# Optimization experiments

Measured on AMD Instinct MI355X. Metric: run time of the kernel, lower is better.

## Reference

```python
import jax, jax.numpy as jnp
import numpy as np

BITS = 8
EPS = 1e-5
NUM_HEADS = 16


def quantize_weight(w, eps=EPS):
    # per-tensor abs-mean scale, ternary weights in {-1, 0, 1}
    scale = jnp.maximum(jnp.mean(jnp.abs(w)), eps)
    qw = jnp.clip(jnp.round(w / scale), -1.0, 1.0)
    return qw, scale


def bitlinear158_inference(x, qw, scale, bias=None, bits=BITS, eps=EPS):
    # per-token abs-max activation quantization to [-Q, Q-1]
    q = float(2 ** (bits - 1))
    gamma = jnp.maximum(jnp.max(jnp.abs(x), axis=-1, keepdims=True), eps)
    qx = jnp.clip(jnp.round(x * (q / gamma)), -q, q - 1.0)
    out = jnp.einsum('...i,oi->...o', qx, qw)
    out = out * (scale * gamma / q)
    if bias is not None:
        out = out + bias
    return out


def setup_inputs() -> dict:
    rng = jax.random.key(0)
    ks = jax.random.split(rng, 7)
    B, L, E = 4, 2048, 1024
    return {
        'query': jax.random.normal(ks[0], (B, L, E), jnp.float32),
        'key': jax.random.normal(ks[1], (B, L, E), jnp.float32),
        'value': jax.random.normal(ks[2], (B, L, E), jnp.float32),
        'in_proj_weight': jax.random.normal(ks[3], (3 * E, E), jnp.float32) * 0.02,
        'in_proj_bias': jax.random.normal(ks[4], (3 * E,), jnp.float32) * 0.02,
        'out_proj_weight': jax.random.normal(ks[5], (E, E), jnp.float32) * 0.02,
        'out_proj_bias': jax.random.normal(ks[6], (E,), jnp.float32) * 0.02,
    }


def reference(query, key, value, in_proj_weight, in_proj_bias, out_proj_weight, out_proj_bias):
    B, Lq, E = query.shape
    Lk = key.shape[1]
    H = NUM_HEADS
    D = E // H

    # quantize weights as done at __init__ time
    qw, kw, vw = jnp.split(in_proj_weight, 3, axis=0)  # each [E, E]
    qb, kb, vb = jnp.split(in_proj_bias, 3, axis=0)
    q_qw, q_s = quantize_weight(qw)
    k_qw, k_s = quantize_weight(kw)
    v_qw, v_s = quantize_weight(vw)
    o_qw, o_s = quantize_weight(out_proj_weight)

    # quantized projections [B, L, E]
    q = bitlinear158_inference(query, q_qw, q_s, qb)
    k = bitlinear158_inference(key, k_qw, k_s, kb)
    v = bitlinear158_inference(value, v_qw, v_s, vb)

    # [B, H, L, D]
    q = q.reshape(B, Lq, H, D).transpose(0, 2, 1, 3)
    k = k.reshape(B, Lk, H, D).transpose(0, 2, 1, 3)
    v = v.reshape(B, Lk, H, D).transpose(0, 2, 1, 3)

    scores = jnp.einsum('bhqd,bhkd->bhqk', q, k) / jnp.sqrt(jnp.asarray(D, q.dtype))
    attn = jax.nn.softmax(scores, axis=-1)
    ctx = jnp.einsum('bhqk,bhkd->bhqd', attn, v)  # [B, H, Lq, D]
    ctx = ctx.transpose(0, 2, 1, 3).reshape(B, Lq, E)

    out = bitlinear158_inference(ctx, o_qw, o_s, out_proj_bias)
    return out
```

## Files before the change

### kernel.cpp

```cpp
#include <hip/hip_runtime.h>
#include <cstdint>
#include <cstddef>

#define BB 4
#define LL 2048
#define EE 1024
#define HH 16
#define DD 64
#define TT (BB*LL)
#define EPSF 1e-5f

typedef _Float16 half8 __attribute__((ext_vector_type(8)));
typedef _Float16 half4v __attribute__((ext_vector_type(4)));
typedef float floatx4 __attribute__((ext_vector_type(4)));
typedef float floatx16 __attribute__((ext_vector_type(16)));
typedef int intx4 __attribute__((ext_vector_type(4)));
typedef unsigned int uintx4 __attribute__((ext_vector_type(4)));

__device__ __forceinline__ void gl_lds16(const void* g, void* l) {
    __builtin_amdgcn_global_load_lds(
        (const __attribute__((address_space(1))) void*)g,
        (__attribute__((address_space(3))) void*)l, 16, 0, 0);
}

__device__ __forceinline__ uint32_t pk2(float a, float b) {
    union { _Float16 h[2]; uint32_t u; } x;
    x.h[0] = (_Float16)a; x.h[1] = (_Float16)b;
    return x.u;
}

__global__ void k_absum(const float* __restrict__ in_proj,
                        const float* __restrict__ out_proj,
                        double* __restrict__ sums) {
    const int which = blockIdx.y;
    const float* src = (which < 3) ? (in_proj + (size_t)which * EE * EE) : out_proj;
    double loc = 0.0;
    const int n = EE * EE;
    for (int i = blockIdx.x * blockDim.x + threadIdx.x; i < n; i += gridDim.x * blockDim.x)
        loc += (double)fabsf(src[i]);
    #pragma unroll
    for (int off = 32; off > 0; off >>= 1) loc += __shfl_down(loc, off, 64);
    __shared__ double red[4];
    const int lane = threadIdx.x & 63, wv = threadIdx.x >> 6;
    if (lane == 0) red[wv] = loc;
    __syncthreads();
    if (threadIdx.x == 0) {
        double tot = red[0] + red[1] + red[2] + red[3];
        atomicAdd(&sums[which], tot);
    }
}

__global__ void k_quantw(const float* __restrict__ in_proj,
                         const float* __restrict__ out_proj,
                         const double* __restrict__ sums,
                         float* __restrict__ scaleF,
                         int8_t* __restrict__ qw) {
    const int idx = blockIdx.x * blockDim.x + threadIdx.x;
    if (idx < 4) scaleF[idx] = fmaxf((float)(sums[idx] * (1.0 / (EE * EE))), EPSF);
    const int which = idx >> 20;
    const float s = fmaxf((float)(sums[which] * (1.0 / (EE * EE))), EPSF);
    const float w = (which < 3) ? in_proj[idx] : out_proj[idx - 3 * EE * EE];
    float q = rintf(w / s);
    q = fminf(fmaxf(q, -1.f), 1.f);
    qw[idx] = (int8_t)q;
}

__global__ __launch_bounds__(256) void k_gammaq(const float* __restrict__ x,
                                                float* __restrict__ g,
                                                int8_t* __restrict__ qx) {
    const int wv = threadIdx.x >> 6, lane = threadIdx.x & 63;
    const int tok = blockIdx.x * 4 + wv;
    const float* xp = x + (size_t)tok * EE;
    float4 v[4];
    #pragma unroll
    for (int i = 0; i < 4; i++) v[i] = *(const float4*)(xp + (lane + 64 * i) * 4);
    float m = 0.f;
    #pragma unroll
    for (int i = 0; i < 4; i++)
        m = fmaxf(m, fmaxf(fmaxf(fabsf(v[i].x), fabsf(v[i].y)),
                           fmaxf(fabsf(v[i].z), fabsf(v[i].w))));
    #pragma unroll
    for (int off = 1; off < 64; off <<= 1) m = fmaxf(m, __shfl_xor(m, off, 64));
    const float gg = fmaxf(m, EPSF);
    const float rg = 128.f / gg;
    int8_t* qp = qx + (size_t)tok * EE;
    #pragma unroll
    for (int i = 0; i < 4; i++) {
        char4 c;
        c.x = (int8_t)(int)fminf(fmaxf(rintf(v[i].x * rg), -128.f), 127.f);
        c.y = (int8_t)(int)fminf(fmaxf(rintf(v[i].y * rg), -128.f), 127.f);
        c.z = (int8_t)(int)fminf(fmaxf(rintf(v[i].z * rg), -128.f), 127.f);
        c.w = (int8_t)(int)fminf(fmaxf(rintf(v[i].w * rg), -128.f), 127.f);
        *(char4*)(qp + (lane + 64 * i) * 4) = c;
    }
    if (lane == 0) g[tok] = gg;
}

__global__ __launch_bounds__(256) void k_bitmm(
    const int8_t* __restrict__ qx, const float* __restrict__ gam,
    const int8_t* __restrict__ qw, const float* __restrict__ scaleF, int widx,
    const float* __restrict__ bias, float* __restrict__ outF,
    _Float16* __restrict__ outH, int mode, float pre) {
    __shared__ __align__(16) int8_t smem[36864];
    int8_t (*As)[128] = (int8_t(*)[128])smem;
    int8_t (*Bs)[128] = (int8_t(*)[128])(smem + 16384);
    _Float16 (*Vt)[136] = (_Float16(*)[136])smem;
    const int tid = threadIdx.x;
    const int wv = tid >> 6, lane = tid & 63;
    const int quad = lane >> 4, l16 = lane & 15;
    const int wm = wv & 1, wn = wv >> 1;
    const int t0 = blockIdx.x * 128, o0 = blockIdx.y * 128;
    const int srow = lane >> 3, schunk = lane & 7;
    const int cc = schunk ^ srow;

    intx4 acc[4][4];
    #pragma unroll
    for (int i = 0; i < 4; i++)
        #pragma unroll
        for (int j = 0; j < 4; j++) acc[i][j] = (intx4){0, 0, 0, 0};

    for (int k0 = 0; k0 < EE; k0 += 128) {
        __syncthreads();
        #pragma unroll
        for (int p = 0; p < 4; p++) {
            const int row = wv * 32 + p * 8 + srow;
            gl_lds16(qx + (size_t)(t0 + row) * EE + k0 + cc * 16, &As[wv * 32 + p * 8][0]);
            gl_lds16(qw + (size_t)(o0 + row) * EE + k0 + cc * 16, &Bs[wv * 32 + p * 8][0]);
        }
        __syncthreads();
        #pragma unroll
        for (int kk = 0; kk < 2; kk++) {
            intx4 af[4], bf[4];
            #pragma unroll
            for (int s4 = 0; s4 < 4; s4++) {
                const int ph = ((kk * 4 + quad) ^ (l16 & 7)) * 16;
                af[s4] = *(const intx4*)&As[wm * 64 + s4 * 16 + l16][ph];
                bf[s4] = *(const intx4*)&Bs[wn * 64 + s4 * 16 + l16][ph];
            }
            #pragma unroll
            for (int sm = 0; sm < 4; sm++)
                #pragma unroll
                for (int sn = 0; sn < 4; sn++)
                    acc[sm][sn] = __builtin_amdgcn_mfma_i32_16x16x64_i8(
                        af[sm], bf[sn], acc[sm][sn], 0, 0, 0);
        }
    }

    const float s = scaleF[widx];
    if (mode == 2) {
        __syncthreads();
        #pragma unroll
        for (int sm = 0; sm < 4; sm++) {
            const int tl = wm * 64 + sm * 16 + quad * 4;
            float mr[4];
            #pragma unroll
            for (int r = 0; r < 4; r++) mr[r] = s * gam[t0 + tl + r] * 0.0078125f;
            #pragma unroll
            for (int sn = 0; sn < 4; sn++) {
                const int ol = wn * 64 + sn * 16 + l16;
                const float b = bias[o0 + ol];
                half4v hv;
                #pragma unroll
                for (int r = 0; r < 4; r++)
                    hv[r] = (_Float16)((float)acc[sm][sn][r] * mr[r] + b);
                *(half4v*)&Vt[ol][tl] = hv;
            }
        }
        __syncthreads();
        const int ol2 = tid >> 1, tc0 = (tid & 1) * 64;
        const int og = o0 + ol2, hh = og >> 6, dd = og & 63;
        const int bb = t0 >> 11, l0 = t0 & (LL - 1);
        _Float16* dst = outH + ((size_t)(bb * HH + hh) * DD + dd) * LL + l0 + tc0;
        #pragma unroll
        for (int i = 0; i < 8; i++)
            *(half8*)(dst + i * 8) = *(const half8*)&Vt[ol2][tc0 + i * 8];
        return;
    }
    #pragma unroll
    for (int sm = 0; sm < 4; sm++) {
        #pragma unroll
        for (int r = 0; r < 4; r++) {
            const int t = t0 + wm * 64 + sm * 16 + quad * 4 + r;
            const float mr = s * gam[t] * 0.0078125f;
            const int b_ = t >> 11, l_ = t & (LL - 1);
            #pragma unroll
            for (int sn = 0; sn < 4; sn++) {
                const int o = o0 + wn * 64 + sn * 16 + l16;
                const float val = (float)acc[sm][sn][r] * mr + bias[o];
                if (mode == 0) {
                    outF[(size_t)t * EE + o] = val;
                } else {
                    const int h_ = o >> 6, d_ = o & 63;
                    outH[((size_t)(b_ * HH + h_) * LL + l_) * DD + d_] = (_Float16)(val * pre);
                }
            }
        }
    }
}

__global__ __launch_bounds__(256) void k_attn4(const _Float16* __restrict__ Q,
                                               const _Float16* __restrict__ K,
                                               const _Float16* __restrict__ Vt,
                                               float* __restrict__ ctx) {
    __shared__ __align__(16) _Float16 Ksh[64][64];
    __shared__ __align__(16) _Float16 Vtsh[64][64];
    const int tid = threadIdx.x;
    const int wv = tid >> 6, lane = tid & 63;
    const int l32 = lane & 31, h2 = lane >> 5;
    const int bh = blockIdx.y, b_ = bh >> 4, h_ = bh & 15;
    const int q0 = blockIdx.x * 256 + wv * 64;
    const int srow = lane >> 3, schunk = lane & 7;
    const int cc = schunk ^ srow;

    const _Float16* Qb = Q + (size_t)bh * LL * DD;
    const _Float16* Kb = K + (size_t)bh * LL * DD;
    const _Float16* Vtb = Vt + (size_t)bh * DD * LL;

    half8 qf[2][4];
    #pragma unroll
    for (int qh = 0; qh < 2; qh++)
        #pragma unroll
        for (int ds = 0; ds < 4; ds++)
            qf[qh][ds] = *(const half8*)(Qb + (size_t)(q0 + qh * 32 + l32) * DD + ds * 16 + h2 * 8);

    floatx16 acc[2][2];
    #pragma unroll
    for (int r = 0; r < 16; r++) {
        acc[0][0][r] = 0.f; acc[0][1][r] = 0.f; acc[1][0][r] = 0.f; acc[1][1][r] = 0.f;
    }
    float lsum[2] = {0.f, 0.f};

    for (int kt = 0; kt < LL; kt += 64) {
        __syncthreads();
        #pragma unroll
        for (int u = 0; u < 2; u++) {
            const int row = wv * 16 + u * 8 + srow;
            gl_lds16(Kb + (size_t)(kt + row) * DD + cc * 8, &Ksh[wv * 16 + u * 8][0]);
            gl_lds16(Vtb + (size_t)row * LL + kt + cc * 8, &Vtsh[wv * 16 + u * 8][0]);
        }
        __syncthreads();

        half8 pa[4][2];
        #pragma unroll
        for (int ks = 0; ks < 2; ks++) {
            const int rowK = ks * 32 + l32;
            const int mK = l32 & 7;
            half8 kf[4];
            #pragma unroll
            for (int ds = 0; ds < 4; ds++)
                kf[ds] = *(const half8*)&Ksh[rowK][((2 * ds + h2) ^ mK) * 8];
            #pragma unroll
            for (int qh = 0; qh < 2; qh++) {
                floatx16 sc;
                #pragma unroll
                for (int r = 0; r < 16; r++) sc[r] = 0.f;
                #pragma unroll
                for (int ds = 0; ds < 4; ds++)
                    sc = __builtin_amdgcn_mfma_f32_32x32x16_f16(kf[ds], qf[qh][ds], sc, 0, 0, 0);
                float p[16];
                #pragma unroll
                for (int r = 0; r < 16; r++) p[r] = __builtin_amdgcn_exp2f(sc[r]);
                #pragma unroll
                for (int r = 0; r < 16; r++) lsum[qh] += p[r];
                uint32_t u_[4][2], o_[4][2];
                #pragma unroll
                for (int c4 = 0; c4 < 4; c4++) {
                    u_[c4][0] = pk2(p[4 * c4 + 0], p[4 * c4 + 1]);
                    u_[c4][1] = pk2(p[4 * c4 + 2], p[4 * c4 + 3]);
                    o_[c4][0] = __shfl_xor(u_[c4][0], 32, 64);
                    o_[c4][1] = __shfl_xor(u_[c4][1], 32, 64);
                }
                #pragma unroll
                for (int mm = 0; mm < 2; mm++) {
                    const uint32_t ua = h2 ? u_[2 * mm + 1][0] : u_[2 * mm][0];
                    const uint32_t ub = h2 ? u_[2 * mm + 1][1] : u_[2 * mm][1];
                    const uint32_t oa = h2 ? o_[2 * mm + 1][0] : o_[2 * mm][0];
                    const uint32_t ob = h2 ? o_[2 * mm + 1][1] : o_[2 * mm][1];
                    uintx4 w;
                    w[0] = h2 ? oa : ua;  w[1] = h2 ? ob : ub;
                    w[2] = h2 ? ua : oa;  w[3] = h2 ? ub : ob;
                    union { uintx4 u; half8 h; } cv; cv.u = w;
                    pa[ks * 2 + mm][qh] = cv.h;
                }
            }
        }

        #pragma unroll
        for (int kb = 0; kb < 4; kb++) {
            #pragma unroll
            for (int sd = 0; sd < 2; sd++) {
                const int rowV = sd * 32 + l32;
                const half8 vf = *(const half8*)&Vtsh[rowV][((2 * kb + h2) ^ (l32 & 7)) * 8];
                #pragma unroll
                for (int qh = 0; qh < 2; qh++)
                    acc[qh][sd] = __builtin_amdgcn_mfma_f32_32x32x16_f16(
                        pa[kb][qh], vf, acc[qh][sd], 0, 0, 0);
            }
        }
    }

    float invl[2];
    #pragma unroll
    for (int qh = 0; qh < 2; qh++) {
        lsum[qh] += __shfl_xor(lsum[qh], 32, 64);
        invl[qh] = 1.f / lsum[qh];
    }
    #pragma unroll
    for (int qh = 0; qh < 2; qh++)
        #pragma unroll
        for (int r = 0; r < 16; r++) {
            const int qrow = (r & 3) + 8 * (r >> 2) + 4 * h2;
            const float iv = __shfl(invl[qh], qrow, 64);
            float* cp = ctx + ((size_t)b_ * LL + q0 + qh * 32 + qrow) * EE + h_ * DD + l32;
            cp[0]  = acc[qh][0][r] * iv;
            cp[32] = acc[qh][1][r] * iv;
        }
}

extern "C" void kernel_launch(void* const* d_in, const int* in_sizes, int n_in,
                              void* d_out, int out_size, void* d_ws, size_t ws_size,
                              hipStream_t stream) {
    const float* query      = (const float*)d_in[0];
    const float* key        = (const float*)d_in[1];
    const float* value      = (const float*)d_in[2];
    const float* in_proj_w  = (const float*)d_in[3];
    const float* in_proj_b  = (const float*)d_in[4];
    const float* out_proj_w = (const float*)d_in[5];
    const float* out_proj_b = (const float*)d_in[6];
    float* out = (float*)d_out;

    char* ws = (char*)d_ws;
    double*   sums   = (double*)ws;
    float*    scaleF = (float*)(ws + 32);
    float*    gbuf   = (float*)(ws + 256);
    int8_t*   qw8    = (int8_t*)(ws + (size_t)1  * 1024 * 1024);
    int8_t*   qx8    = (int8_t*)(ws + (size_t)8  * 1024 * 1024);
    _Float16* Qh     = (_Float16*)(ws + (size_t)40 * 1024 * 1024);
    _Float16* Kh     = Qh + (size_t)TT * EE;
    _Float16* Vth    = Kh + (size_t)TT * EE;
    float*    ctx    = out;

    const float QPRE = 0.18033688011112042f;

    hipMemsetAsync(sums, 0, 32, stream);
    k_absum<<<dim3(64, 4), 256, 0, stream>>>(in_proj_w, out_proj_w, sums);
    k_quantw<<<(4 * EE * EE) / 256, 256, 0, stream>>>(in_proj_w, out_proj_w, sums, scaleF, qw8);
    k_gammaq<<<TT / 4, 256, 0, stream>>>(query, gbuf + 0 * TT, qx8 + 0 * (size_t)TT * EE);
    k_gammaq<<<TT / 4, 256, 0, stream>>>(key,   gbuf + 1 * TT, qx8 + 1 * (size_t)TT * EE);
    k_gammaq<<<TT / 4, 256, 0, stream>>>(value, gbuf + 2 * TT, qx8 + 2 * (size_t)TT * EE);

    dim3 gg(TT / 128, EE / 128);
    k_bitmm<<<gg, 256, 0, stream>>>(qx8 + 0 * (size_t)TT * EE, gbuf + 0 * TT,
                                    qw8 + 0 * (size_t)EE * EE, scaleF, 0,
                                    in_proj_b + 0,    nullptr, Qh, 1, QPRE);
    k_bitmm<<<gg, 256, 0, stream>>>(qx8 + 1 * (size_t)TT * EE, gbuf + 1 * TT,
                                    qw8 + 1 * (size_t)EE * EE, scaleF, 1,
                                    in_proj_b + 1024, nullptr, Kh, 1, 1.0f);
    k_bitmm<<<gg, 256, 0, stream>>>(qx8 + 2 * (size_t)TT * EE, gbuf + 2 * TT,
                                    qw8 + 2 * (size_t)EE * EE, scaleF, 2,
                                    in_proj_b + 2048, nullptr, Vth, 2, 1.0f);

    k_attn4<<<dim3(LL / 256, BB * HH), 256, 0, stream>>>(Qh, Kh, Vth, ctx);

    k_gammaq<<<TT / 4, 256, 0, stream>>>(ctx, gbuf + 3 * TT, qx8 + 3 * (size_t)TT * EE);
    k_bitmm<<<gg, 256, 0, stream>>>(qx8 + 3 * (size_t)TT * EE, gbuf + 3 * TT,
                                    qw8 + 3 * (size_t)EE * EE, scaleF, 3,
                                    out_proj_b, out, nullptr, 0, 1.0f);
}
```

Before: 368.6 us.

## Batch QKV launches, rework LDS swizzle, and halve attention rows per wave

Merges the three activation-quantization launches and the three QKV projection GEMMs into single launches indexed by grid y/z, cutting launch overhead and tail effects. Changes the LDS XOR swizzle in both the GEMM and attention loads to also mix in the row-group index, aiming to reduce bank conflicts. Attention now handles 32 query rows per wave instead of 64, with a min-blocks launch bound of 4, doubling the grid for more occupancy. The trade-off is that K/V tiles are reused across fewer query rows, so LDS fill traffic per unit of compute goes up.

```diff
diff --git a/kernel.cpp b/kernel.cpp
--- a/kernel.cpp
+++ b/kernel.cpp
@@ -65,9 +65,9 @@
     qw[idx] = (int8_t)q;
 }
 
-__global__ __launch_bounds__(256) void k_gammaq(const float* __restrict__ x,
-                                                float* __restrict__ g,
-                                                int8_t* __restrict__ qx) {
+__device__ __forceinline__ void gammaq_body(const float* __restrict__ x,
+                                            float* __restrict__ g,
+                                            int8_t* __restrict__ qx) {
     const int wv = threadIdx.x >> 6, lane = threadIdx.x & 63;
     const int tok = blockIdx.x * 4 + wv;
     const float* xp = x + (size_t)tok * EE;
@@ -96,22 +96,45 @@
     if (lane == 0) g[tok] = gg;
 }
 
+__global__ __launch_bounds__(256) void k_gammaq3(const float* __restrict__ q,
+                                                 const float* __restrict__ k,
+                                                 const float* __restrict__ v,
+                                                 float* __restrict__ g,
+                                                 int8_t* __restrict__ qx) {
+    const int y = blockIdx.y;
+    const float* src = (y == 0) ? q : (y == 1) ? k : v;
+    gammaq_body(src, g + (size_t)y * TT, qx + (size_t)y * TT * EE);
+}
+
+__global__ __launch_bounds__(256) void k_gammaq(const float* __restrict__ x,
+                                                float* __restrict__ g,
+                                                int8_t* __restrict__ qx) {
+    gammaq_body(x, g, qx);
+}
+
 __global__ __launch_bounds__(256) void k_bitmm(
-    const int8_t* __restrict__ qx, const float* __restrict__ gam,
-    const int8_t* __restrict__ qw, const float* __restrict__ scaleF, int widx,
-    const float* __restrict__ bias, float* __restrict__ outF,
-    _Float16* __restrict__ outH, int mode, float pre) {
+    const int8_t* __restrict__ qx_all, const float* __restrict__ gam_all,
+    const int8_t* __restrict__ qw_all, const float* __restrict__ scaleF,
+    const float* __restrict__ in_proj_b, const float* __restrict__ out_proj_b,
+    float* __restrict__ outF, _Float16* __restrict__ outH_all,
+    int wbase, float qpre) {
     __shared__ __align__(16) int8_t smem[36864];
     int8_t (*As)[128] = (int8_t(*)[128])smem;
     int8_t (*Bs)[128] = (int8_t(*)[128])(smem + 16384);
     _Float16 (*Vt)[136] = (_Float16(*)[136])smem;
+    const int widx = wbase + blockIdx.z;
+    const int8_t* qx = qx_all + (size_t)widx * TT * EE;
+    const int8_t* qw = qw_all + (size_t)widx * EE * EE;
+    const float* gam = gam_all + (size_t)widx * TT;
+    const float* bias = (widx < 3) ? (in_proj_b + widx * EE) : out_proj_b;
+    _Float16* outH = outH_all + (size_t)widx * TT * EE;
+    const float pre = (widx == 0) ? qpre : 1.0f;
     const int tid = threadIdx.x;
     const int wv = tid >> 6, lane = tid & 63;
     const int quad = lane >> 4, l16 = lane & 15;
     const int wm = wv & 1, wn = wv >> 1;
     const int t0 = blockIdx.x * 128, o0 = blockIdx.y * 128;
     const int srow = lane >> 3, schunk = lane & 7;
-    const int cc = schunk ^ srow;
 
     intx4 acc[4][4];
     #pragma unroll
@@ -123,9 +146,11 @@
         __syncthreads();
         #pragma unroll
         for (int p = 0; p < 4; p++) {
-            const int row = wv * 32 + p * 8 + srow;
-            gl_lds16(qx + (size_t)(t0 + row) * EE + k0 + cc * 16, &As[wv * 32 + p * 8][0]);
-            gl_lds16(qw + (size_t)(o0 + row) * EE + k0 + cc * 16, &Bs[wv * 32 + p * 8][0]);
+            const int g = wv * 4 + p;
+            const int c = schunk ^ srow ^ (g & 7);
+            const int row = g * 8 + srow;
+            gl_lds16(qx + (size_t)(t0 + row) * EE + k0 + c * 16, &As[g * 8][0]);
+            gl_lds16(qw + (size_t)(o0 + row) * EE + k0 + c * 16, &Bs[g * 8][0]);
         }
         __syncthreads();
         #pragma unroll
@@ -133,7 +158,8 @@
             intx4 af[4], bf[4];
             #pragma unroll
             for (int s4 = 0; s4 < 4; s4++) {
-                const int ph = ((kk * 4 + quad) ^ (l16 & 7)) * 16;
+                const int mR = (l16 & 7) ^ ((s4 * 2 + (l16 >> 3)) & 7);
+                const int ph = ((kk * 4 + quad) ^ mR) * 16;
                 af[s4] = *(const intx4*)&As[wm * 64 + s4 * 16 + l16][ph];
                 bf[s4] = *(const intx4*)&Bs[wn * 64 + s4 * 16 + l16][ph];
             }
@@ -147,7 +173,7 @@
     }
 
     const float s = scaleF[widx];
-    if (mode == 2) {
+    if (widx == 2) {
         __syncthreads();
         #pragma unroll
         for (int sm = 0; sm < 4; sm++) {
@@ -187,7 +213,7 @@
             for (int sn = 0; sn < 4; sn++) {
                 const int o = o0 + wn * 64 + sn * 16 + l16;
                 const float val = (float)acc[sm][sn][r] * mr + bias[o];
-                if (mode == 0) {
+                if (widx == 3) {
                     outF[(size_t)t * EE + o] = val;
                 } else {
                     const int h_ = o >> 6, d_ = o & 63;
@@ -198,90 +224,82 @@
     }
 }
 
-__global__ __launch_bounds__(256) void k_attn4(const _Float16* __restrict__ Q,
-                                               const _Float16* __restrict__ K,
-                                               const _Float16* __restrict__ Vt,
-                                               float* __restrict__ ctx) {
+__global__ __launch_bounds__(256, 4) void k_attn5(const _Float16* __restrict__ Q,
+                                                  const _Float16* __restrict__ K,
+                                                  const _Float16* __restrict__ Vt,
+                                                  float* __restrict__ ctx) {
     __shared__ __align__(16) _Float16 Ksh[64][64];
     __shared__ __align__(16) _Float16 Vtsh[64][64];
     const int tid = threadIdx.x;
     const int wv = tid >> 6, lane = tid & 63;
     const int l32 = lane & 31, h2 = lane >> 5;
     const int bh = blockIdx.y, b_ = bh >> 4, h_ = bh & 15;
-    const int q0 = blockIdx.x * 256 + wv * 64;
+    const int q0 = blockIdx.x * 128 + wv * 32;
     const int srow = lane >> 3, schunk = lane & 7;
-    const int cc = schunk ^ srow;
 
     const _Float16* Qb = Q + (size_t)bh * LL * DD;
     const _Float16* Kb = K + (size_t)bh * LL * DD;
     const _Float16* Vtb = Vt + (size_t)bh * DD * LL;
 
-    half8 qf[2][4];
-    #pragma unroll
-    for (int qh = 0; qh < 2; qh++)
-        #pragma unroll
-        for (int ds = 0; ds < 4; ds++)
-            qf[qh][ds] = *(const half8*)(Qb + (size_t)(q0 + qh * 32 + l32) * DD + ds * 16 + h2 * 8);
-
-    floatx16 acc[2][2];
-    #pragma unroll
-    for (int r = 0; r < 16; r++) {
-        acc[0][0][r] = 0.f; acc[0][1][r] = 0.f; acc[1][0][r] = 0.f; acc[1][1][r] = 0.f;
-    }
-    float lsum[2] = {0.f, 0.f};
+    half8 qf[4];
+    #pragma unroll
+    for (int ds = 0; ds < 4; ds++)
+        qf[ds] = *(const half8*)(Qb + (size_t)(q0 + l32) * DD + ds * 16 + h2 * 8);
+
+    floatx16 acc[2];
+    #pragma unroll
+    for (int r = 0; r < 16; r++) { acc[0][r] = 0.f; acc[1][r] = 0.f; }
+    float lsum = 0.f;
 
     for (int kt = 0; kt < LL; kt += 64) {
         __syncthreads();
         #pragma unroll
         for (int u = 0; u < 2; u++) {
-            const int row = wv * 16 + u * 8 + srow;
-            gl_lds16(Kb + (size_t)(kt + row) * DD + cc * 8, &Ksh[wv * 16 + u * 8][0]);
-            gl_lds16(Vtb + (size_t)row * LL + kt + cc * 8, &Vtsh[wv * 16 + u * 8][0]);
-        }
-        __syncthreads();
-
-        half8 pa[4][2];
+            const int g = wv * 2 + u;
+            const int c = schunk ^ srow ^ (g & 7);
+            const int row = g * 8 + srow;
+            gl_lds16(Kb + (size_t)(kt + row) * DD + c * 8, &Ksh[g * 8][0]);
+            gl_lds16(Vtb + (size_t)row * LL + kt + c * 8, &Vtsh[g * 8][0]);
+        }
+        __syncthreads();
+
+        half8 pa[4];
         #pragma unroll
         for (int ks = 0; ks < 2; ks++) {
             const int rowK = ks * 32 + l32;
-            const int mK = l32 & 7;
-            half8 kf[4];
-            #pragma unroll
-            for (int ds = 0; ds < 4; ds++)
-                kf[ds] = *(const half8*)&Ksh[rowK][((2 * ds + h2) ^ mK) * 8];
-            #pragma unroll
-            for (int qh = 0; qh < 2; qh++) {
-                floatx16 sc;
-                #pragma unroll
-                for (int r = 0; r < 16; r++) sc[r] = 0.f;
-                #pragma unroll
-                for (int ds = 0; ds < 4; ds++)
-                    sc = __builtin_amdgcn_mfma_f32_32x32x16_f16(kf[ds], qf[qh][ds], sc, 0, 0, 0);
-                float p[16];
-                #pragma unroll
-                for (int r = 0; r < 16; r++) p[r] = __builtin_amdgcn_exp2f(sc[r]);
-                #pragma unroll
-                for (int r = 0; r < 16; r++) lsum[qh] += p[r];
-                uint32_t u_[4][2], o_[4][2];
-                #pragma unroll
-                for (int c4 = 0; c4 < 4; c4++) {
-                    u_[c4][0] = pk2(p[4 * c4 + 0], p[4 * c4 + 1]);
-                    u_[c4][1] = pk2(p[4 * c4 + 2], p[4 * c4 + 3]);
-                    o_[c4][0] = __shfl_xor(u_[c4][0], 32, 64);
-                    o_[c4][1] = __shfl_xor(u_[c4][1], 32, 64);
-                }
-                #pragma unroll
-                for (int mm = 0; mm < 2; mm++) {
-                    const uint32_t ua = h2 ? u_[2 * mm + 1][0] : u_[2 * mm][0];
-                    const uint32_t ub = h2 ? u_[2 * mm + 1][1] : u_[2 * mm][1];
-                    const uint32_t oa = h2 ? o_[2 * mm + 1][0] : o_[2 * mm][0];
-                    const uint32_t ob = h2 ? o_[2 * mm + 1][1] : o_[2 * mm][1];
-                    uintx4 w;
-                    w[0] = h2 ? oa : ua;  w[1] = h2 ? ob : ub;
-                    w[2] = h2 ? ua : oa;  w[3] = h2 ? ub : ob;
-                    union { uintx4 u; half8 h; } cv; cv.u = w;
-                    pa[ks * 2 + mm][qh] = cv.h;
-                }
+            const int mK = (l32 & 7) ^ ((ks * 4 + (l32 >> 3)) & 7);
+            floatx16 sc;
+            #pragma unroll
+            for (int r = 0; r < 16; r++) sc[r] = 0.f;
+            #pragma unroll
+            for (int ds = 0; ds < 4; ds++) {
+                const half8 kf = *(const half8*)&Ksh[rowK][((2 * ds + h2) ^ mK) * 8];
+                sc = __builtin_amdgcn_mfma_f32_32x32x16_f16(kf, qf[ds], sc, 0, 0, 0);
+            }
+            float p[16];
+            #pragma unroll
+            for (int r = 0; r < 16; r++) p[r] = __builtin_amdgcn_exp2f(sc[r]);
+            #pragma unroll
+            for (int r = 0; r < 16; r++) lsum += p[r];
+            uint32_t u_[4][2], o_[4][2];
+            #pragma unroll
+            for (int c4 = 0; c4 < 4; c4++) {
+                u_[c4][0] = pk2(p[4 * c4 + 0], p[4 * c4 + 1]);
+                u_[c4][1] = pk2(p[4 * c4 + 2], p[4 * c4 + 3]);
+                o_[c4][0] = __shfl_xor(u_[c4][0], 32, 64);
+                o_[c4][1] = __shfl_xor(u_[c4][1], 32, 64);
+            }
+            #pragma unroll
+            for (int mm = 0; mm < 2; mm++) {
+                const uint32_t ua = h2 ? u_[2 * mm + 1][0] : u_[2 * mm][0];
+                const uint32_t ub = h2 ? u_[2 * mm + 1][1] : u_[2 * mm][1];
+                const uint32_t oa = h2 ? o_[2 * mm + 1][0] : o_[2 * mm][0];
+                const uint32_t ob = h2 ? o_[2 * mm + 1][1] : o_[2 * mm][1];
+                uintx4 w;
+                w[0] = h2 ? oa : ua;  w[1] = h2 ? ob : ub;
+                w[2] = h2 ? ua : oa;  w[3] = h2 ? ub : ob;
+                union { uintx4 u; half8 h; } cv; cv.u = w;
+                pa[ks * 2 + mm] = cv.h;
             }
         }
 
@@ -290,31 +308,23 @@
             #pragma unroll
             for (int sd = 0; sd < 2; sd++) {
                 const int rowV = sd * 32 + l32;
-                const half8 vf = *(const half8*)&Vtsh[rowV][((2 * kb + h2) ^ (l32 & 7)) * 8];
-                #pragma unroll
-                for (int qh = 0; qh < 2; qh++)
-                    acc[qh][sd] = __builtin_amdgcn_mfma_f32_32x32x16_f16(
-                        pa[kb][qh], vf, acc[qh][sd], 0, 0, 0);
-            }
-        }
-    }
-
-    float invl[2];
-    #pragma unroll
-    for (int qh = 0; qh < 2; qh++) {
-        lsum[qh] += __shfl_xor(lsum[qh], 32, 64);
-        invl[qh] = 1.f / lsum[qh];
-    }
-    #pragma unroll
-    for (int qh = 0; qh < 2; qh++)
-        #pragma unroll
-        for (int r = 0; r < 16; r++) {
-            const int qrow = (r & 3) + 8 * (r >> 2) + 4 * h2;
-            const float iv = __shfl(invl[qh], qrow, 64);
-            float* cp = ctx + ((size_t)b_ * LL + q0 + qh * 32 + qrow) * EE + h_ * DD + l32;
-            cp[0]  = acc[qh][0][r] * iv;
-            cp[32] = acc[qh][1][r] * iv;
-        }
+                const int mV = (l32 & 7) ^ ((sd * 4 + (l32 >> 3)) & 7);
+                const half8 vf = *(const half8*)&Vtsh[rowV][((2 * kb + h2) ^ mV) * 8];
+                acc[sd] = __builtin_amdgcn_mfma_f32_32x32x16_f16(pa[kb], vf, acc[sd], 0, 0, 0);
+            }
+        }
+    }
+
+    lsum += __shfl_xor(lsum, 32, 64);
+    const float invl = 1.f / lsum;
+    #pragma unroll
+    for (int r = 0; r < 16; r++) {
+        const int qrow = (r & 3) + 8 * (r >> 2) + 4 * h2;
+        const float iv = __shfl(invl, qrow, 64);
+        float* cp = ctx + ((size_t)b_ * LL + q0 + qrow) * EE + h_ * DD + l32;
+        cp[0]  = acc[0][r] * iv;
+        cp[32] = acc[1][r] * iv;
+    }
 }
 
 extern "C" void kernel_launch(void* const* d_in, const int* in_sizes, int n_in,
@@ -345,25 +355,14 @@
     hipMemsetAsync(sums, 0, 32, stream);
     k_absum<<<dim3(64, 4), 256, 0, stream>>>(in_proj_w, out_proj_w, sums);
     k_quantw<<<(4 * EE * EE) / 256, 256, 0, stream>>>(in_proj_w, out_proj_w, sums, scaleF, qw8);
-    k_gammaq<<<TT / 4, 256, 0, stream>>>(query, gbuf + 0 * TT, qx8 + 0 * (size_t)TT * EE);
-    k_gammaq<<<TT / 4, 256, 0, stream>>>(key,   gbuf + 1 * TT, qx8 + 1 * (size_t)TT * EE);
-    k_gammaq<<<TT / 4, 256, 0, stream>>>(value, gbuf + 2 * TT, qx8 + 2 * (size_t)TT * EE);
-
-    dim3 gg(TT / 128, EE / 128);
-    k_bitmm<<<gg, 256, 0, stream>>>(qx8 + 0 * (size_t)TT * EE, gbuf + 0 * TT,
-                                    qw8 + 0 * (size_t)EE * EE, scaleF, 0,
-                                    in_proj_b + 0,    nullptr, Qh, 1, QPRE);
-    k_bitmm<<<gg, 256, 0, stream>>>(qx8 + 1 * (size_t)TT * EE, gbuf + 1 * TT,
-                                    qw8 + 1 * (size_t)EE * EE, scaleF, 1,
-                                    in_proj_b + 1024, nullptr, Kh, 1, 1.0f);
-    k_bitmm<<<gg, 256, 0, stream>>>(qx8 + 2 * (size_t)TT * EE, gbuf + 2 * TT,
-                                    qw8 + 2 * (size_t)EE * EE, scaleF, 2,
-                                    in_proj_b + 2048, nullptr, Vth, 2, 1.0f);
-
-    k_attn4<<<dim3(LL / 256, BB * HH), 256, 0, stream>>>(Qh, Kh, Vth, ctx);
+    k_gammaq3<<<dim3(TT / 4, 3), 256, 0, stream>>>(query, key, value, gbuf, qx8);
+
+    k_bitmm<<<dim3(TT / 128, EE / 128, 3), 256, 0, stream>>>(
+        qx8, gbuf, qw8, scaleF, in_proj_b, out_proj_b, nullptr, Qh, 0, QPRE);
+
+    k_attn5<<<dim3(LL / 128, BB * HH), 256, 0, stream>>>(Qh, Kh, Vth, ctx);
 
     k_gammaq<<<TT / 4, 256, 0, stream>>>(ctx, gbuf + 3 * TT, qx8 + 3 * (size_t)TT * EE);
-    k_bitmm<<<gg, 256, 0, stream>>>(qx8 + 3 * (size_t)TT * EE, gbuf + 3 * TT,
-                                    qw8 + 3 * (size_t)EE * EE, scaleF, 3,
-                                    out_proj_b, out, nullptr, 0, 1.0f);
-}
+    k_bitmm<<<dim3(TT / 128, EE / 128, 1), 256, 0, stream>>>(
+        qx8, gbuf, qw8, scaleF, in_proj_b, out_proj_b, out, Qh, 3, QPRE);
+}
```

Result: faster. 355.4 us (-3.6%).
